# Performance work log

Measured on AMD Instinct MI355X. Metric: run time of the kernel, lower is better.

The kernel has to match this reference:

```python
import jax, jax.numpy as jnp
from jax import lax
import numpy as np

D_MODEL, D_STATE, EXPAND, D_CONV = 1024, 16, 2, 4
D_INNER = EXPAND * D_MODEL
B, L = 4, 2048


def setup_inputs() -> dict:
    key = jax.random.key(0)
    ks = jax.random.split(key, 12)
    def xavier(k, shape):
        fan_in, fan_out = shape[1], shape[0]
        lim = float(np.sqrt(6.0 / (fan_in + fan_out)))
        return jax.random.uniform(k, shape, jnp.float32, -lim, lim)
    inp = {}
    inp['x'] = jax.random.normal(ks[0], (B, L, D_MODEL), jnp.float32)
    inp['W_left'] = xavier(ks[1], (D_INNER, D_MODEL))
    inp['conv_w'] = jax.random.normal(ks[2], (D_INNER, 1, D_CONV), jnp.float32) * (1.0 / np.sqrt(D_CONV))
    inp['conv_b'] = jax.random.normal(ks[3], (D_INNER,), jnp.float32) * 0.01
    inp['W_delta'] = jax.random.normal(ks[4], (D_INNER, D_INNER), jnp.float32) * (1.0 / np.sqrt(D_INNER))
    inp['b_delta'] = jnp.zeros((D_INNER,), jnp.float32)
    inp['W_B'] = jax.random.normal(ks[5], (D_STATE, D_INNER), jnp.float32) * (1.0 / np.sqrt(D_INNER))
    inp['W_C'] = jax.random.normal(ks[6], (D_STATE, D_INNER), jnp.float32) * (1.0 / np.sqrt(D_INNER))
    inp['A_log'] = jnp.log(jnp.arange(1, D_STATE + 1, dtype=jnp.float32))
    inp['W_right'] = xavier(ks[7], (D_INNER, D_MODEL))
    inp['ln_g'] = jnp.ones((D_INNER,), jnp.float32)
    inp['ln_b'] = jnp.zeros((D_INNER,), jnp.float32)
    inp['W_out'] = xavier(ks[8], (D_MODEL, D_INNER))
    return inp


def _ssm(xl, W_delta, b_delta, W_B, W_C, A_log):
    # xl: [b, l, d_inner]
    b, l, d_inner = xl.shape
    A = -jax.nn.softplus(A_log)  # [d_state]
    delta = jnp.clip(jax.nn.softplus(xl @ W_delta.T + b_delta), 1e-4, 10.0)
    Bm = xl @ W_B.T  # [b, l, d_state]
    Cm = xl @ W_C.T  # [b, l, d_state]

    def step(h, inp):
        d_t, x_t, B_t, C_t = inp  # [b,d_inner], [b,d_inner], [b,N], [b,N]
        A_bar = jnp.exp(d_t[:, :, None] * A)            # [b, d_inner, N]
        h = A_bar * h + (d_t * x_t)[:, :, None] * B_t[:, None, :]
        y_t = jnp.einsum('bdn,bn->bd', h, C_t)
        return h, y_t

    h0 = jnp.zeros((b, d_inner, A_log.shape[0]), xl.dtype)
    xs = (jnp.swapaxes(delta, 0, 1), jnp.swapaxes(xl, 0, 1),
          jnp.swapaxes(Bm, 0, 1), jnp.swapaxes(Cm, 0, 1))
    _, ys = lax.scan(step, h0, xs)  # ys: [l, b, d_inner]
    return jnp.swapaxes(ys, 0, 1)


def reference(x, W_left, conv_w, conv_b, W_delta, b_delta, W_B, W_C, A_log,
              W_right, ln_g, ln_b, W_out):
    d_conv = conv_w.shape[-1]
    # left branch: linear -> causal depthwise conv1d -> silu
    left = x @ W_left.T                          # [b, l, d_inner]
    left_ncw = jnp.swapaxes(left, 1, 2)          # [b, d_inner, l]
    left_ncw = jnp.pad(left_ncw, ((0, 0), (0, 0), (d_conv - 1, 0)))
    left_ncw = lax.conv_general_dilated(
        left_ncw, conv_w, window_strides=(1,), padding='VALID',
        feature_group_count=conv_w.shape[0]) + conv_b[None, :, None]
    left = jax.nn.silu(jnp.swapaxes(left_ncw, 1, 2))
    # selective scan
    ssm_out = _ssm(left, W_delta, b_delta, W_B, W_C, A_log)
    # right gate (eval mode: dropout off)
    gate = jax.nn.silu(x @ W_right.T)
    out = ssm_out * gate
    # layernorm over d_inner
    mu = jnp.mean(out, axis=-1, keepdims=True)
    var = jnp.mean(jnp.square(out - mu), axis=-1, keepdims=True)
    out = (out - mu) * lax.rsqrt(var + 1e-5) * ln_g + ln_b
    return out @ W_out.T
```

## Files before the change

### kernel.cpp

```cpp
#include <hip/hip_runtime.h>
#include <cstddef>

#define LL 2048
#define TOK 8192
#define DM 1024
#define DI 2048
#define NS 16

typedef _Float16 half_t;
typedef __attribute__((ext_vector_type(8))) _Float16 f16x8;
typedef __attribute__((ext_vector_type(4))) _Float16 f16x4;
typedef __attribute__((ext_vector_type(4))) float f32x4;

__device__ __forceinline__ float softplus_f(float x) {
  return fmaxf(x, 0.f) + log1pf(__expf(-fabsf(x)));
}
__device__ __forceinline__ float silu_f(float x) {
  return x / (1.f + __expf(-x));
}
__device__ __forceinline__ void gload_lds16(const void* g, void* l) {
  __builtin_amdgcn_global_load_lds((const __attribute__((address_space(1))) void*)g,
                                   (__attribute__((address_space(3))) void*)l, 16, 0, 0);
}
#define DPP_ADD(v, ctrl) \
  ((v) + __int_as_float(__builtin_amdgcn_update_dpp(0, __float_as_int(v), (ctrl), 0xf, 0xf, true)))

__device__ float g_buf[120881152];

__global__ __launch_bounds__(256) void f2h_k(const float* __restrict__ in,
                                             half_t* __restrict__ out, int n4) {
  const int i = blockIdx.x * 256 + threadIdx.x;
  if (i >= n4) return;
  const float4 v = ((const float4*)in)[i];
  f16x4 o;
  o[0] = (half_t)v.x; o[1] = (half_t)v.y; o[2] = (half_t)v.z; o[3] = (half_t)v.w;
  ((f16x4*)out)[i] = o;
}

__global__ __launch_bounds__(256) void f2h2_k(const float* __restrict__ in,
                                              half_t* __restrict__ hi,
                                              half_t* __restrict__ lo, int n4) {
  const int i = blockIdx.x * 256 + threadIdx.x;
  if (i >= n4) return;
  const float4 v = ((const float4*)in)[i];
  f16x4 h, l;
  h[0] = (half_t)v.x; h[1] = (half_t)v.y; h[2] = (half_t)v.z; h[3] = (half_t)v.w;
  l[0] = (half_t)(v.x - (float)h[0]);
  l[1] = (half_t)(v.y - (float)h[1]);
  l[2] = (half_t)(v.z - (float)h[2]);
  l[3] = (half_t)(v.w - (float)h[3]);
  ((f16x4*)hi)[i] = h;
  ((f16x4*)lo)[i] = l;
}

template <int ACT>
__global__ __launch_bounds__(256) void gemm_mfma(const half_t* __restrict__ A,
                                                 const half_t* __restrict__ W,
                                                 const float* __restrict__ bias,
                                                 float* __restrict__ C,
                                                 int M, int N, int K) {
  __shared__ half_t lA[4096];
  __shared__ half_t lB[4096];
  const int tid = threadIdx.x;
  const int bm0 = blockIdx.y * 128, bn0 = blockIdx.x * 128;
  const int lane = tid & 63, wave = tid >> 6;
  const int q = lane >> 4, mr = lane & 15;
  const int wm = (wave >> 1) * 64, wn = (wave & 1) * 64;
  const int flat0 = tid, flat1 = tid + 256;
  const int kc0 = flat0 >> 7, r0 = flat0 & 127;
  const int kc1 = flat1 >> 7, r1 = flat1 & 127;

  f32x4 acc[4][4];
#pragma unroll
  for (int i = 0; i < 4; ++i)
#pragma unroll
    for (int j = 0; j < 4; ++j) acc[i][j] = (f32x4){0.f, 0.f, 0.f, 0.f};

  for (int k0 = 0; k0 < K; k0 += 32) {
    gload_lds16(A + (size_t)(bm0 + r0) * K + k0 + kc0 * 8, lA + (size_t)flat0 * 8);
    gload_lds16(A + (size_t)(bm0 + r1) * K + k0 + kc1 * 8, lA + (size_t)flat1 * 8);
    gload_lds16(W + (size_t)(bn0 + r0) * K + k0 + kc0 * 8, lB + (size_t)flat0 * 8);
    gload_lds16(W + (size_t)(bn0 + r1) * K + k0 + kc1 * 8, lB + (size_t)flat1 * 8);
    __syncthreads();
    f16x8 af[4], bg[4];
#pragma unroll
    for (int t = 0; t < 4; ++t) {
      af[t] = *(const f16x8*)(lA + ((q << 10) + ((wm + t * 16 + mr) << 3)));
      bg[t] = *(const f16x8*)(lB + ((q << 10) + ((wn + t * 16 + mr) << 3)));
    }
#pragma unroll
    for (int i = 0; i < 4; ++i)
#pragma unroll
      for (int j = 0; j < 4; ++j)
        acc[i][j] = __builtin_amdgcn_mfma_f32_16x16x32_f16(af[i], bg[j], acc[i][j], 0, 0, 0);
    __syncthreads();
  }

#pragma unroll
  for (int i = 0; i < 4; ++i) {
#pragma unroll
    for (int j = 0; j < 4; ++j) {
      const int col = bn0 + wn + j * 16 + mr;
      const float bv = bias ? bias[col] : 0.f;
#pragma unroll
      for (int r = 0; r < 4; ++r) {
        const int row = bm0 + wm + i * 16 + q * 4 + r;
        float v = acc[i][j][r] + bv;
        if (ACT == 1) v = silu_f(v);
        C[(size_t)row * N + col] = v;
      }
    }
  }
}

__global__ __launch_bounds__(256) void gemm_mfma_split(const half_t* __restrict__ Ah,
                                                       const half_t* __restrict__ Wh,
                                                       const half_t* __restrict__ Wl,
                                                       const float* __restrict__ bias,
                                                       float* __restrict__ C,
                                                       int M, int N, int K) {
  __shared__ half_t lAh[4096], lBh[4096], lBl[4096];
  const int tid = threadIdx.x;
  const int bm0 = blockIdx.y * 128, bn0 = blockIdx.x * 128;
  const int lane = tid & 63, wave = tid >> 6;
  const int q = lane >> 4, mr = lane & 15;
  const int wm = (wave >> 1) * 64, wn = (wave & 1) * 64;
  const int flat0 = tid, flat1 = tid + 256;
  const int kc0 = flat0 >> 7, r0 = flat0 & 127;
  const int kc1 = flat1 >> 7, r1 = flat1 & 127;

  f32x4 acc[4][4];
#pragma unroll
  for (int i = 0; i < 4; ++i)
#pragma unroll
    for (int j = 0; j < 4; ++j) acc[i][j] = (f32x4){0.f, 0.f, 0.f, 0.f};

  for (int k0 = 0; k0 < K; k0 += 32) {
    const size_t ga0 = (size_t)(bm0 + r0) * K + k0 + kc0 * 8;
    const size_t ga1 = (size_t)(bm0 + r1) * K + k0 + kc1 * 8;
    const size_t gb0 = (size_t)(bn0 + r0) * K + k0 + kc0 * 8;
    const size_t gb1 = (size_t)(bn0 + r1) * K + k0 + kc1 * 8;
    gload_lds16(Ah + ga0, lAh + (size_t)flat0 * 8);
    gload_lds16(Ah + ga1, lAh + (size_t)flat1 * 8);
    gload_lds16(Wh + gb0, lBh + (size_t)flat0 * 8);
    gload_lds16(Wh + gb1, lBh + (size_t)flat1 * 8);
    gload_lds16(Wl + gb0, lBl + (size_t)flat0 * 8);
    gload_lds16(Wl + gb1, lBl + (size_t)flat1 * 8);
    __syncthreads();
    f16x8 ah[4], bh[4], bl[4];
#pragma unroll
    for (int t = 0; t < 4; ++t) {
      const int ao = (q << 10) + ((wm + t * 16 + mr) << 3);
      const int bo = (q << 10) + ((wn + t * 16 + mr) << 3);
      ah[t] = *(const f16x8*)(lAh + ao);
      bh[t] = *(const f16x8*)(lBh + bo);
      bl[t] = *(const f16x8*)(lBl + bo);
    }
#pragma unroll
    for (int i = 0; i < 4; ++i)
#pragma unroll
      for (int j = 0; j < 4; ++j) {
        acc[i][j] = __builtin_amdgcn_mfma_f32_16x16x32_f16(ah[i], bh[j], acc[i][j], 0, 0, 0);
        acc[i][j] = __builtin_amdgcn_mfma_f32_16x16x32_f16(ah[i], bl[j], acc[i][j], 0, 0, 0);
      }
    __syncthreads();
  }

#pragma unroll
  for (int i = 0; i < 4; ++i) {
#pragma unroll
    for (int j = 0; j < 4; ++j) {
      const int col = bn0 + wn + j * 16 + mr;
      const float bv = bias[col];
#pragma unroll
      for (int r = 0; r < 4; ++r) {
        const int row = bm0 + wm + i * 16 + q * 4 + r;
        float v = softplus_f(acc[i][j][r] + bv);
        v = fminf(fmaxf(v, 1e-4f), 10.f);
        C[(size_t)row * N + col] = v;
      }
    }
  }
}

__global__ __launch_bounds__(256) void bc_mfma(const half_t* __restrict__ A,
                                               const half_t* __restrict__ Wbc,
                                               float* __restrict__ bc) {
  __shared__ half_t lA[4096];
  __shared__ half_t lB[1024];
  const int tid = threadIdx.x;
  const int bm0 = blockIdx.x * 128;
  const int lane = tid & 63, wave = tid >> 6;
  const int q = lane >> 4, mr = lane & 15;
  const int wm = wave * 32;
  const int flat1 = tid + 256;
  const int kcA0 = tid >> 7, rA0 = tid & 127;
  const int kcA1 = flat1 >> 7, rA1 = flat1 & 127;
  const int kcB = tid >> 5, rB = tid & 31;

  f32x4 acc[2][2];
#pragma unroll
  for (int i = 0; i < 2; ++i)
#pragma unroll
    for (int j = 0; j < 2; ++j) acc[i][j] = (f32x4){0.f, 0.f, 0.f, 0.f};

  for (int k0 = 0; k0 < DI; k0 += 32) {
    gload_lds16(A + (size_t)(bm0 + rA0) * DI + k0 + kcA0 * 8, lA + (size_t)tid * 8);
    gload_lds16(A + (size_t)(bm0 + rA1) * DI + k0 + kcA1 * 8, lA + (size_t)flat1 * 8);
    if (tid < 128)
      gload_lds16(Wbc + (size_t)rB * DI + k0 + kcB * 8, lB + (size_t)tid * 8);
    __syncthreads();
    f16x8 af[2], bg[2];
#pragma unroll
    for (int t = 0; t < 2; ++t) {
      af[t] = *(const f16x8*)(lA + ((q << 10) + ((wm + t * 16 + mr) << 3)));
      bg[t] = *(const f16x8*)(lB + ((q << 8) + ((t * 16 + mr) << 3)));
    }
#pragma unroll
    for (int i = 0; i < 2; ++i)
#pragma unroll
      for (int j = 0; j < 2; ++j)
        acc[i][j] = __builtin_amdgcn_mfma_f32_16x16x32_f16(af[i], bg[j], acc[i][j], 0, 0, 0);
    __syncthreads();
  }

#pragma unroll
  for (int i = 0; i < 2; ++i) {
#pragma unroll
    for (int j = 0; j < 2; ++j) {
#pragma unroll
      for (int r = 0; r < 4; ++r) {
        const int row = bm0 + wm + i * 16 + q * 4 + r;
        bc[(size_t)row * 32 + 2 * mr + j] = acc[i][j][r];
      }
    }
  }
}

__global__ __launch_bounds__(256) void conv_silu_k(const float* __restrict__ left,
                                                   const float* __restrict__ cw,
                                                   const float* __restrict__ cb,
                                                   float* __restrict__ xc,
                                                   half_t* __restrict__ xch) {
  const int idx = blockIdx.x * 256 + threadIdx.x;
  const int d = idx & (DI - 1);
  const int bt = idx >> 11;
  const int t = bt & (LL - 1);
  const float4 wv = *(const float4*)(cw + (size_t)d * 4);
  float acc = cb[d];
  const size_t base = (size_t)idx;
  if (t >= 3) {
    acc += left[base - 3 * DI] * wv.x + left[base - 2 * DI] * wv.y +
           left[base - DI] * wv.z + left[base] * wv.w;
  } else {
    acc += left[base] * wv.w;
    if (t >= 1) acc += left[base - DI] * wv.z;
    if (t >= 2) acc += left[base - 2 * DI] * wv.y;
  }
  const float v = silu_f(acc);
  xc[base] = v;
  xch[base] = (half_t)v;
}

#define ST 32
__global__ __launch_bounds__(256) void scan_k(const float* __restrict__ delta,
                                              const float* __restrict__ xc,
                                              const float* __restrict__ gate,
                                              const float* __restrict__ bcp,
                                              const float* __restrict__ A_log,
                                              float* __restrict__ y) {
  __shared__ float dx2[16 * 68];
  __shared__ float bcs[ST * 32];
  __shared__ float ys[ST * 16];
  const int tid = threadIdx.x;
  const int b  = blockIdx.x >> 7;
  const int d0 = (blockIdx.x & 127) << 4;
  const int n  = tid & 15;
  const int ch = tid >> 4;
  const float An = -softplus_f(A_log[n]);

  const int t_a = tid >> 4, c_a = tid & 15;
  const int t_b = t_a + 16;

  float h = 0.f;
  const size_t batch_base = (size_t)b * LL * DI + d0;
  const size_t batch_bc   = (size_t)b * LL * 32;

  size_t rb_cur = batch_base;
  float g0, g1;
  {
    const size_t ra = rb_cur + (size_t)t_a * DI + c_a;
    const size_t rbx = rb_cur + (size_t)t_b * DI + c_a;
    const float d0v = delta[ra], x0v = xc[ra];
    const float d1v = delta[rbx], x1v = xc[rbx];
    g0 = gate[ra]; g1 = gate[rbx];
    const float2 b0 = *(const float2*)&bcp[batch_bc + (size_t)t_a * 32 + 2 * c_a];
    const float2 b1 = *(const float2*)&bcp[batch_bc + (size_t)t_b * 32 + 2 * c_a];
    *(float2*)&dx2[c_a * 68 + t_a * 2] = make_float2(d0v, x0v);
    *(float2*)&dx2[c_a * 68 + t_b * 2] = make_float2(d1v, x1v);
    *(float2*)&bcs[t_a * 32 + 2 * c_a] = b0;
    *(float2*)&bcs[t_b * 32 + 2 * c_a] = b1;
  }
  __syncthreads();

  for (int it = 0; it < LL / ST; ++it) {
    float nd0, nx0, ng0, nd1, nx1, ng1;
    float2 nb0, nb1;
    const size_t rb_nxt = batch_base + (size_t)(it + 1) * ST * DI;
    if (it + 1 < LL / ST) {
      const size_t ra = rb_nxt + (size_t)t_a * DI + c_a;
      const size_t rbx = rb_nxt + (size_t)t_b * DI + c_a;
      nd0 = delta[ra]; nx0 = xc[ra]; ng0 = gate[ra];
      nd1 = delta[rbx]; nx1 = xc[rbx]; ng1 = gate[rbx];
      const size_t bcb = batch_bc + (size_t)(it + 1) * ST * 32;
      nb0 = *(const float2*)&bcp[bcb + (size_t)t_a * 32 + 2 * c_a];
      nb1 = *(const float2*)&bcp[bcb + (size_t)t_b * 32 + 2 * c_a];
    }

    const float* dxp = &dx2[ch * 68];
#pragma unroll
    for (int tt = 0; tt < ST; tt += 2) {
      const float4 v = *(const float4*)&dxp[tt * 2];
      const float2 bc0 = *(const float2*)&bcs[tt * 32 + 2 * n];
      const float2 bc1 = *(const float2*)&bcs[(tt + 1) * 32 + 2 * n];
      float ab = __expf(v.x * An);
      h = fmaf(ab, h, v.x * v.y * bc0.x);
      float p = h * bc0.y;
      p = DPP_ADD(p, 0x111); p = DPP_ADD(p, 0x112);
      p = DPP_ADD(p, 0x114); p = DPP_ADD(p, 0x118);
      if (n == 15) ys[tt * 16 + ch] = p;
      ab = __expf(v.z * An);
      h = fmaf(ab, h, v.z * v.w * bc1.x);
      p = h * bc1.y;
      p = DPP_ADD(p, 0x111); p = DPP_ADD(p, 0x112);
      p = DPP_ADD(p, 0x114); p = DPP_ADD(p, 0x118);
      if (n == 15) ys[(tt + 1) * 16 + ch] = p;
    }
    __syncthreads();

    if (it + 1 < LL / ST) {
      *(float2*)&dx2[c_a * 68 + t_a * 2] = make_float2(nd0, nx0);
      *(float2*)&dx2[c_a * 68 + t_b * 2] = make_float2(nd1, nx1);
      *(float2*)&bcs[t_a * 32 + 2 * c_a] = nb0;
      *(float2*)&bcs[t_b * 32 + 2 * c_a] = nb1;
    }
    y[rb_cur + (size_t)t_a * DI + c_a] = ys[t_a * 16 + c_a] * g0;
    y[rb_cur + (size_t)t_b * DI + c_a] = ys[t_b * 16 + c_a] * g1;
    g0 = ng0; g1 = ng1;
    rb_cur = rb_nxt;
    __syncthreads();
  }
}

__global__ __launch_bounds__(256) void ln_k(const float* __restrict__ y,
                                            const float* __restrict__ gam,
                                            const float* __restrict__ bet,
                                            half_t* __restrict__ outn) {
  const int row = blockIdx.x;
  const int tid = threadIdx.x;
  const float* yr = y + (size_t)row * DI;
  const float4 v0 = ((const float4*)yr)[tid];
  const float4 v1 = ((const float4*)yr)[tid + 256];
  float s = v0.x + v0.y + v0.z + v0.w + v1.x + v1.y + v1.z + v1.w;
  float q = v0.x * v0.x + v0.y * v0.y + v0.z * v0.z + v0.w * v0.w +
            v1.x * v1.x + v1.y * v1.y + v1.z * v1.z + v1.w * v1.w;
  for (int off = 32; off > 0; off >>= 1) {
    s += __shfl_down(s, off);
    q += __shfl_down(q, off);
  }
  __shared__ float sred[4], qred[4];
  const int wid = tid >> 6;
  if ((tid & 63) == 0) { sred[wid] = s; qred[wid] = q; }
  __syncthreads();
  s = sred[0] + sred[1] + sred[2] + sred[3];
  q = qred[0] + qred[1] + qred[2] + qred[3];
  const float mu = s * (1.f / DI);
  const float rs = rsqrtf(q * (1.f / DI) - mu * mu + 1e-5f);
  half_t* orow = outn + (size_t)row * DI;
  const int c0 = tid * 4, c1 = (tid + 256) * 4;
  f16x4 o;
  o[0] = (half_t)((v0.x - mu) * rs * gam[c0 + 0] + bet[c0 + 0]);
  o[1] = (half_t)((v0.y - mu) * rs * gam[c0 + 1] + bet[c0 + 1]);
  o[2] = (half_t)((v0.z - mu) * rs * gam[c0 + 2] + bet[c0 + 2]);
  o[3] = (half_t)((v0.w - mu) * rs * gam[c0 + 3] + bet[c0 + 3]);
  ((f16x4*)orow)[tid] = o;
  o[0] = (half_t)((v1.x - mu) * rs * gam[c1 + 0] + bet[c1 + 0]);
  o[1] = (half_t)((v1.y - mu) * rs * gam[c1 + 1] + bet[c1 + 1]);
  o[2] = (half_t)((v1.z - mu) * rs * gam[c1 + 2] + bet[c1 + 2]);
  o[3] = (half_t)((v1.w - mu) * rs * gam[c1 + 3] + bet[c1 + 3]);
  ((f16x4*)orow)[tid + 256] = o;
}

extern "C" void kernel_launch(void* const* d_in, const int* in_sizes, int n_in,
                              void* d_out, int out_size, void* d_ws, size_t ws_size,
                              hipStream_t stream) {
  const float* x       = (const float*)d_in[0];
  const float* W_left  = (const float*)d_in[1];
  const float* conv_w  = (const float*)d_in[2];
  const float* conv_b  = (const float*)d_in[3];
  const float* W_delta = (const float*)d_in[4];
  const float* b_delta = (const float*)d_in[5];
  const float* W_B     = (const float*)d_in[6];
  const float* W_C     = (const float*)d_in[7];
  const float* A_log   = (const float*)d_in[8];
  const float* W_right = (const float*)d_in[9];
  const float* ln_g    = (const float*)d_in[10];
  const float* ln_b    = (const float*)d_in[11];
  const float* W_out   = (const float*)d_in[12];

  float* buf = nullptr;
  hipGetSymbolAddress((void**)&buf, HIP_SYMBOL(g_buf));
  half_t* xh   = (half_t*)(buf + 0);
  half_t* wlh  = (half_t*)(buf + 4194304);
  half_t* wrh  = (half_t*)(buf + 5242880);
  half_t* wdh  = (half_t*)(buf + 6291456);
  half_t* wdl  = (half_t*)(buf + 8388608);
  half_t* woh  = (half_t*)(buf + 10485760);
  float* left  = buf + 11534336;
  float* xc    = buf + 28311552;
  half_t* xch  = (half_t*)(buf + 45088768);
  float* dlt   = buf + 61865984;
  float* gate  = buf + 78643200;
  float* yv    = buf + 95420416;
  half_t* nrmh = (half_t*)(buf + 112197632);
  float* bc    = buf + 120586240;
  half_t* wbch = (half_t*)(buf + 120848384);

  f2h_k<<<8192, 256, 0, stream>>>(x, xh, TOK * DM / 4);
  f2h_k<<<2048, 256, 0, stream>>>(W_left, wlh, DI * DM / 4);
  f2h_k<<<2048, 256, 0, stream>>>(W_right, wrh, DI * DM / 4);
  f2h_k<<<2048, 256, 0, stream>>>(W_out, woh, DM * DI / 4);
  f2h2_k<<<4096, 256, 0, stream>>>(W_delta, wdh, wdl, DI * DI / 4);
  f2h_k<<<32, 256, 0, stream>>>(W_B, wbch, NS * DI / 4);
  f2h_k<<<32, 256, 0, stream>>>(W_C, wbch + NS * DI, NS * DI / 4);

  gemm_mfma<0><<<dim3(DI / 128, TOK / 128), 256, 0, stream>>>(xh, wlh, nullptr, left, TOK, DI, DM);
  conv_silu_k<<<TOK * DI / 256, 256, 0, stream>>>(left, conv_w, conv_b, xc, xch);
  gemm_mfma<1><<<dim3(DI / 128, TOK / 128), 256, 0, stream>>>(xh, wrh, nullptr, gate, TOK, DI, DM);
  gemm_mfma_split<<<dim3(DI / 128, TOK / 128), 256, 0, stream>>>(xch, wdh, wdl, b_delta, dlt, TOK, DI, DI);
  bc_mfma<<<TOK / 128, 256, 0, stream>>>(xch, wbch, bc);
  scan_k<<<512, 256, 0, stream>>>(dlt, xc, gate, bc, A_log, yv);
  ln_k<<<TOK, 256, 0, stream>>>(yv, ln_g, ln_b, nrmh);
  gemm_mfma<0><<<dim3(DM / 128, TOK / 128), 256, 0, stream>>>(nrmh, woh, nullptr, (float*)d_out, TOK, DM, DI);
}
```

Baseline: 990.5 us.

## Fuse left/gate projections into one GEMM and enlarge delta GEMM tiles

The left and right input projections become a single GEMM launch, gemm_mfma_lg. It works over the contiguous half-precision W_left/W_right buffer, and each block picks its output, plain or SiLU-gated, from its column index. The split-precision delta GEMM now uses 256x128 tiles with 512 threads, so each loaded hi/lo weight tile serves twice as many rows. This aims to cut launch overhead and global weight traffic. The larger block and the launch-bounds occupancy hint may raise register pressure and lower occupancy.

```diff
diff --git a/kernel.cpp b/kernel.cpp
--- a/kernel.cpp
+++ b/kernel.cpp
@@ -113,20 +113,20 @@
   }
 }
 
-__global__ __launch_bounds__(256) void gemm_mfma_split(const half_t* __restrict__ Ah,
-                                                       const half_t* __restrict__ Wh,
-                                                       const half_t* __restrict__ Wl,
-                                                       const float* __restrict__ bias,
-                                                       float* __restrict__ C,
-                                                       int M, int N, int K) {
-  __shared__ half_t lAh[4096], lBh[4096], lBl[4096];
+__global__ __launch_bounds__(256) void gemm_mfma_lg(const half_t* __restrict__ A,
+                                                    const half_t* __restrict__ W,
+                                                    float* __restrict__ left,
+                                                    float* __restrict__ gate) {
+  __shared__ half_t lA[4096];
+  __shared__ half_t lB[4096];
   const int tid = threadIdx.x;
   const int bm0 = blockIdx.y * 128, bn0 = blockIdx.x * 128;
+  const int K = DM;
   const int lane = tid & 63, wave = tid >> 6;
   const int q = lane >> 4, mr = lane & 15;
   const int wm = (wave >> 1) * 64, wn = (wave & 1) * 64;
-  const int flat0 = tid, flat1 = tid + 256;
-  const int kc0 = flat0 >> 7, r0 = flat0 & 127;
+  const int flat1 = tid + 256;
+  const int kc0 = tid >> 7, r0 = tid & 127;
   const int kc1 = flat1 >> 7, r1 = flat1 & 127;
 
   f32x4 acc[4][4];
@@ -136,21 +136,78 @@
     for (int j = 0; j < 4; ++j) acc[i][j] = (f32x4){0.f, 0.f, 0.f, 0.f};
 
   for (int k0 = 0; k0 < K; k0 += 32) {
-    const size_t ga0 = (size_t)(bm0 + r0) * K + k0 + kc0 * 8;
-    const size_t ga1 = (size_t)(bm0 + r1) * K + k0 + kc1 * 8;
-    const size_t gb0 = (size_t)(bn0 + r0) * K + k0 + kc0 * 8;
-    const size_t gb1 = (size_t)(bn0 + r1) * K + k0 + kc1 * 8;
-    gload_lds16(Ah + ga0, lAh + (size_t)flat0 * 8);
-    gload_lds16(Ah + ga1, lAh + (size_t)flat1 * 8);
-    gload_lds16(Wh + gb0, lBh + (size_t)flat0 * 8);
-    gload_lds16(Wh + gb1, lBh + (size_t)flat1 * 8);
-    gload_lds16(Wl + gb0, lBl + (size_t)flat0 * 8);
-    gload_lds16(Wl + gb1, lBl + (size_t)flat1 * 8);
+    gload_lds16(A + (size_t)(bm0 + r0) * K + k0 + kc0 * 8, lA + (size_t)tid * 8);
+    gload_lds16(A + (size_t)(bm0 + r1) * K + k0 + kc1 * 8, lA + (size_t)flat1 * 8);
+    gload_lds16(W + (size_t)(bn0 + r0) * K + k0 + kc0 * 8, lB + (size_t)tid * 8);
+    gload_lds16(W + (size_t)(bn0 + r1) * K + k0 + kc1 * 8, lB + (size_t)flat1 * 8);
+    __syncthreads();
+    f16x8 af[4], bg[4];
+#pragma unroll
+    for (int t = 0; t < 4; ++t) {
+      af[t] = *(const f16x8*)(lA + ((q << 10) + ((wm + t * 16 + mr) << 3)));
+      bg[t] = *(const f16x8*)(lB + ((q << 10) + ((wn + t * 16 + mr) << 3)));
+    }
+#pragma unroll
+    for (int i = 0; i < 4; ++i)
+#pragma unroll
+      for (int j = 0; j < 4; ++j)
+        acc[i][j] = __builtin_amdgcn_mfma_f32_16x16x32_f16(af[i], bg[j], acc[i][j], 0, 0, 0);
+    __syncthreads();
+  }
+
+  const int is_gate = (bn0 >= DI);
+  float* out = is_gate ? gate : left;
+  const int cb = bn0 - (is_gate ? DI : 0);
+#pragma unroll
+  for (int i = 0; i < 4; ++i) {
+#pragma unroll
+    for (int j = 0; j < 4; ++j) {
+      const int col = cb + wn + j * 16 + mr;
+#pragma unroll
+      for (int r = 0; r < 4; ++r) {
+        const int row = bm0 + wm + i * 16 + q * 4 + r;
+        float v = acc[i][j][r];
+        if (is_gate) v = silu_f(v);
+        out[(size_t)row * DI + col] = v;
+      }
+    }
+  }
+}
+
+__global__ __launch_bounds__(512, 4) void gemm_mfma_split(const half_t* __restrict__ Ah,
+                                                          const half_t* __restrict__ Wh,
+                                                          const half_t* __restrict__ Wl,
+                                                          const float* __restrict__ bias,
+                                                          float* __restrict__ C,
+                                                          int M, int N, int K) {
+  __shared__ half_t lAh[8192];
+  __shared__ half_t lBh[4096], lBl[4096];
+  const int tid = threadIdx.x;
+  const int bm0 = blockIdx.y * 256, bn0 = blockIdx.x * 128;
+  const int lane = tid & 63, wave = tid >> 6;
+  const int q = lane >> 4, mr = lane & 15;
+  const int wm = (wave >> 1) * 64, wn = (wave & 1) * 64;
+  const int aflat1 = tid + 512;
+  const int akc0 = tid >> 8, ar0 = tid & 255;
+  const int akc1 = aflat1 >> 8, ar1 = aflat1 & 255;
+  const int wkc = tid >> 7, wr = tid & 127;
+
+  f32x4 acc[4][4];
+#pragma unroll
+  for (int i = 0; i < 4; ++i)
+#pragma unroll
+    for (int j = 0; j < 4; ++j) acc[i][j] = (f32x4){0.f, 0.f, 0.f, 0.f};
+
+  for (int k0 = 0; k0 < K; k0 += 32) {
+    gload_lds16(Ah + (size_t)(bm0 + ar0) * K + k0 + akc0 * 8, lAh + (size_t)tid * 8);
+    gload_lds16(Ah + (size_t)(bm0 + ar1) * K + k0 + akc1 * 8, lAh + (size_t)aflat1 * 8);
+    gload_lds16(Wh + (size_t)(bn0 + wr) * K + k0 + wkc * 8, lBh + (size_t)tid * 8);
+    gload_lds16(Wl + (size_t)(bn0 + wr) * K + k0 + wkc * 8, lBl + (size_t)tid * 8);
     __syncthreads();
     f16x8 ah[4], bh[4], bl[4];
 #pragma unroll
     for (int t = 0; t < 4; ++t) {
-      const int ao = (q << 10) + ((wm + t * 16 + mr) << 3);
+      const int ao = (q << 11) + ((wm + t * 16 + mr) << 3);
       const int bo = (q << 10) + ((wn + t * 16 + mr) << 3);
       ah[t] = *(const f16x8*)(lAh + ao);
       bh[t] = *(const f16x8*)(lBh + bo);
@@ -166,6 +223,7 @@
     __syncthreads();
   }
 
+  const int wmg = (wave >> 1) * 64;
 #pragma unroll
   for (int i = 0; i < 4; ++i) {
 #pragma unroll
@@ -174,7 +232,7 @@
       const float bv = bias[col];
 #pragma unroll
       for (int r = 0; r < 4; ++r) {
-        const int row = bm0 + wm + i * 16 + q * 4 + r;
+        const int row = bm0 + wmg + i * 16 + q * 4 + r;
         float v = softplus_f(acc[i][j][r] + bv);
         v = fminf(fmaxf(v, 1e-4f), 10.f);
         C[(size_t)row * N + col] = v;
@@ -411,7 +469,7 @@
   float* buf = nullptr;
   hipGetSymbolAddress((void**)&buf, HIP_SYMBOL(g_buf));
   half_t* xh   = (half_t*)(buf + 0);
-  half_t* wlh  = (half_t*)(buf + 4194304);
+  half_t* wlgh = (half_t*)(buf + 4194304);
   half_t* wrh  = (half_t*)(buf + 5242880);
   half_t* wdh  = (half_t*)(buf + 6291456);
   half_t* wdl  = (half_t*)(buf + 8388608);
@@ -427,17 +485,16 @@
   half_t* wbch = (half_t*)(buf + 120848384);
 
   f2h_k<<<8192, 256, 0, stream>>>(x, xh, TOK * DM / 4);
-  f2h_k<<<2048, 256, 0, stream>>>(W_left, wlh, DI * DM / 4);
+  f2h_k<<<2048, 256, 0, stream>>>(W_left, wlgh, DI * DM / 4);
   f2h_k<<<2048, 256, 0, stream>>>(W_right, wrh, DI * DM / 4);
   f2h_k<<<2048, 256, 0, stream>>>(W_out, woh, DM * DI / 4);
   f2h2_k<<<4096, 256, 0, stream>>>(W_delta, wdh, wdl, DI * DI / 4);
   f2h_k<<<32, 256, 0, stream>>>(W_B, wbch, NS * DI / 4);
   f2h_k<<<32, 256, 0, stream>>>(W_C, wbch + NS * DI, NS * DI / 4);
 
-  gemm_mfma<0><<<dim3(DI / 128, TOK / 128), 256, 0, stream>>>(xh, wlh, nullptr, left, TOK, DI, DM);
+  gemm_mfma_lg<<<dim3(2 * DI / 128, TOK / 128), 256, 0, stream>>>(xh, wlgh, left, gate);
   conv_silu_k<<<TOK * DI / 256, 256, 0, stream>>>(left, conv_w, conv_b, xc, xch);
-  gemm_mfma<1><<<dim3(DI / 128, TOK / 128), 256, 0, stream>>>(xh, wrh, nullptr, gate, TOK, DI, DM);
-  gemm_mfma_split<<<dim3(DI / 128, TOK / 128), 256, 0, stream>>>(xch, wdh, wdl, b_delta, dlt, TOK, DI, DI);
+  gemm_mfma_split<<<dim3(DI / 128, TOK / 256), 512, 0, stream>>>(xch, wdh, wdl, b_delta, dlt, TOK, DI, DI);
   bc_mfma<<<TOK / 128, 256, 0, stream>>>(xch, wbch, bc);
   scan_k<<<512, 256, 0, stream>>>(dlt, xc, gate, bc, A_log, yv);
   ln_k<<<TOK, 256, 0, stream>>>(yv, ln_g, ln_b, nrmh);
```

After: 927.8 us. 1.07x faster.
